# Kernel optimization log

Hardware: AMD Instinct MI355X
Metric: run time of the kernel (lower is better)

Reference implementation:

```python
import jax, jax.numpy as jnp
import numpy as np

H = 4      # n_heads
HD = 32    # head_dim
D = 128    # pair channels = H*HD
S = 384    # sequence length
EPS = 1e-5


def setup_inputs() -> dict:
    key = jax.random.key(0)
    ks = jax.random.split(key, 8)
    return {
        "x": jax.random.normal(ks[0], (1, S, S, D), dtype=jnp.float32),
        "attn_mask": jnp.zeros((1, 1, 1, S), dtype=jnp.float32),
        "ln_w": jax.random.uniform(ks[1], (D,), dtype=jnp.float32),
        "ln_b": jax.random.normal(ks[2], (D,), dtype=jnp.float32) * 0.02,
        "bias_w": jax.random.normal(ks[3], (H, D), dtype=jnp.float32) * 0.02,
        "qkv_w": jax.random.normal(ks[4], (3 * H * HD, D), dtype=jnp.float32) * 0.02,
        "g_w": jax.random.normal(ks[5], (H * HD, D), dtype=jnp.float32) * 0.02,
        "o_w": jax.random.normal(ks[6], (D, H * HD), dtype=jnp.float32) * 0.02,
    }


def reference(x, attn_mask, ln_w, ln_b, bias_w, qkv_w, g_w, o_w):
    # x: [1, S, S, D]; ending=False -> no permute
    xs = x[0]  # [S, S, D]; first S = batch of rows, second S = attended axis
    mu = jnp.mean(xs, axis=-1, keepdims=True)
    var = jnp.mean(jnp.square(xs - mu), axis=-1, keepdims=True)
    ln = (xs - mu) * jax.lax.rsqrt(var + EPS) * ln_w + ln_b  # [S, S, D]

    # triangle bias: D -> H, shaped [1, H, S, S], broadcast over row-batch
    bias = jnp.einsum('ijd,hd->hij', ln, bias_w)  # [H, S, S]

    # fused qkv projection, split heads
    qkv = jnp.einsum('bsd,ed->bse', ln, qkv_w)  # [S, S, 3*H*HD]
    q, k, v = jnp.split(qkv, 3, axis=-1)
    def heads(t):
        return t.reshape(S, S, H, HD).transpose(0, 2, 1, 3)  # [S, H, S, HD]
    q, k, v = heads(q), heads(k), heads(v)

    scale = 1.0 / jnp.sqrt(jnp.float32(HD))
    scores = jnp.einsum('bhqd,bhkd->bhqk', q, k) * scale  # [S, H, S, S]
    scores = scores + bias[None] + attn_mask  # attn_mask broadcasts [1,1,1,S]
    attn = jax.nn.softmax(scores, axis=-1)
    o = jnp.einsum('bhqk,bhkd->bhqd', attn, v)  # [S, H, S, HD]
    o = o.transpose(0, 2, 1, 3).reshape(S, S, H * HD)  # concat heads

    g = jnp.einsum('bsd,ed->bse', ln, g_w)  # [S, S, H*HD]
    o = o * jax.nn.sigmoid(g)
    out = jnp.einsum('bse,de->bsd', o, o_w)  # [S, S, D]
    return out[None]  # [1, S, S, D]
```

## Files before the change

kernel.cpp:

```cpp
#include <hip/hip_runtime.h>
#include <hip/hip_bf16.h>


#define S_ 384
#define D_ 128
#define MTOT (S_*S_)

typedef __bf16 bf16;
typedef __bf16 bf16x8 __attribute__((ext_vector_type(8)));
typedef __bf16 bf16x4 __attribute__((ext_vector_type(4)));
typedef float  f32x4  __attribute__((ext_vector_type(4)));

#define LOG2E      1.4426950408889634f
#define QSCALE     0.17677669529663687f
#define QSCALE_L2E 0.25505008455121566f

#if defined(__has_builtin)
#  if __has_builtin(__builtin_amdgcn_exp2f)
#    define HAVE_EXP2 1
#  else
#    define HAVE_EXP2 0
#  endif
#else
#  define HAVE_EXP2 0
#endif

#if HAVE_EXP2
#  define BIAS_MUL LOG2E
#  define Q_MUL    QSCALE_L2E
__device__ __forceinline__ float fast_pexp(float x) { return __builtin_amdgcn_exp2f(x); }
#else
#  define BIAS_MUL 1.0f
#  define Q_MUL    QSCALE
__device__ __forceinline__ float fast_pexp(float x) { return __expf(x); }
#endif

#define OFF_LN   0u
#define OFF_Q    37748736u
#define OFF_K    75497472u
#define OFF_V    113246208u
#define OFF_G    150994944u
#define OFF_BIAS 188743680u
#define OFF_W2   191102976u
#define OFF_OWB  191234048u

__global__ __launch_bounds__(256) void k0_convert(const float* __restrict__ qkv_w,
                                                  const float* __restrict__ g_w,
                                                  const float* __restrict__ o_w,
                                                  bf16* __restrict__ W2,
                                                  bf16* __restrict__ o_wb) {
    int idx = blockIdx.x * 256 + threadIdx.x;
    if (idx < 512 * 128) {
        float v = (idx < 384 * 128) ? qkv_w[idx] : g_w[idx - 384 * 128];
        W2[idx] = (bf16)v;
    }
    int idx2 = idx - 512 * 128;
    if (idx2 >= 0 && idx2 < 128 * 128) o_wb[idx2] = (bf16)o_w[idx2];
}

__global__ __launch_bounds__(256) void k1_ln(const float* __restrict__ x,
                                             const float* __restrict__ ln_w,
                                             const float* __restrict__ ln_b,
                                             const float* __restrict__ bias_w,
                                             const float* __restrict__ mask,
                                             bf16* __restrict__ ln_ws,
                                             float* __restrict__ bias_f) {
    int wid = threadIdx.x >> 6, lane = threadIdx.x & 63;
    int grp = lane >> 5, sub = lane & 31;
    int pos = blockIdx.x * 8 + wid * 2 + grp;
    f32x4 v = ((const f32x4*)(x + (size_t)pos * D_))[sub];
    float sum = v[0] + v[1] + v[2] + v[3];
    float ssq = v[0]*v[0] + v[1]*v[1] + v[2]*v[2] + v[3]*v[3];
    #pragma unroll
    for (int off = 16; off; off >>= 1) {
        sum += __shfl_xor(sum, off);
        ssq += __shfl_xor(ssq, off);
    }
    float mu   = sum * (1.0f / D_);
    float var  = ssq * (1.0f / D_) - mu * mu;
    float rstd = rsqrtf(var + 1e-5f);
    f32x4 w4 = ((const f32x4*)ln_w)[sub];
    f32x4 b4 = ((const f32x4*)ln_b)[sub];
    f32x4 y;
    #pragma unroll
    for (int i = 0; i < 4; ++i) y[i] = (v[i] - mu) * rstd * w4[i] + b4[i];
    bf16x4 yb;
    #pragma unroll
    for (int i = 0; i < 4; ++i) yb[i] = (bf16)y[i];
    *(bf16x4*)(ln_ws + (size_t)pos * D_ + 4 * sub) = yb;

    int ii = pos / S_, jj = pos - ii * S_;
    float mk = mask[jj];
    float p[4];
    #pragma unroll
    for (int h = 0; h < 4; ++h) {
        f32x4 bw = ((const f32x4*)(bias_w + h * D_))[sub];
        p[h] = y[0]*bw[0] + y[1]*bw[1] + y[2]*bw[2] + y[3]*bw[3];
    }
    #pragma unroll
    for (int off = 16; off; off >>= 1)
        #pragma unroll
        for (int h = 0; h < 4; ++h) p[h] += __shfl_xor(p[h], off);
    if (sub == 0) {
        int base = ((ii >> 4) * 24 + (jj >> 4)) * 256 + (((jj >> 2) & 3) * 16 + (ii & 15)) * 4 + (jj & 3);
        #pragma unroll
        for (int h = 0; h < 4; ++h)
            bias_f[h * 147456 + base] = (p[h] + mk) * BIAS_MUL;
    }
}

__global__ __launch_bounds__(512, 2) void k2_proj(const bf16* __restrict__ ln_ws,
                                                  const bf16* __restrict__ W2,
                                                  bf16* __restrict__ q_ws,
                                                  bf16* __restrict__ k_ws,
                                                  bf16* __restrict__ v_ws,
                                                  bf16* __restrict__ g_ws) {
    __shared__ __align__(16) char smem[128 * 272 + 128 * 272];
    char* As = smem;
    char* Bs = smem + 128 * 272;
    char* Cs = smem;
    int t = threadIdx.x;
    int bid = blockIdx.x;
    int xcd = bid & 7;
    int rem = bid >> 3;
    int by  = rem & 3;
    int bx  = ((rem >> 2) << 3) + xcd;
    int m0 = bx * 128;
    int n0 = by * 128;
    #pragma unroll
    for (int it = 0; it < 4; ++it) {
        int byte = it * 8192 + t * 16;
        int row = byte >> 8, colb = byte & 255;
        *(int4*)(As + row * 272 + colb) = *(const int4*)((const char*)ln_ws + (size_t)(m0 + row) * 256 + colb);
    }
    #pragma unroll
    for (int it = 0; it < 4; ++it) {
        int byte = it * 8192 + t * 16;
        int row = byte >> 8, colb = byte & 255;
        *(int4*)(Bs + row * 272 + colb) = *(const int4*)((const char*)W2 + (size_t)(n0 + row) * 256 + colb);
    }
    __syncthreads();
    int wid = t >> 6, lane = t & 63, lr = lane & 15, g = lane >> 4;
    int wm = wid >> 1, wn = wid & 1;
    f32x4 acc[2][4] = {};
    #pragma unroll
    for (int ks = 0; ks < 4; ++ks) {
        bf16x8 af[2], bfr[4];
        #pragma unroll
        for (int mt = 0; mt < 2; ++mt)
            af[mt] = *(const bf16x8*)(As + (wm * 32 + mt * 16 + lr) * 272 + ks * 64 + g * 16);
        #pragma unroll
        for (int nt = 0; nt < 4; ++nt)
            bfr[nt] = *(const bf16x8*)(Bs + (wn * 64 + nt * 16 + lr) * 272 + ks * 64 + g * 16);
        #pragma unroll
        for (int mt = 0; mt < 2; ++mt)
            #pragma unroll
            for (int nt = 0; nt < 4; ++nt)
                acc[mt][nt] = __builtin_amdgcn_mfma_f32_16x16x32_bf16(af[mt], bfr[nt], acc[mt][nt], 0, 0, 0);
    }
    __syncthreads();
    float cmul = (by == 0) ? Q_MUL : 1.0f;
    #pragma unroll
    for (int mt = 0; mt < 2; ++mt)
        #pragma unroll
        for (int nt = 0; nt < 4; ++nt)
            #pragma unroll
            for (int i = 0; i < 4; ++i) {
                int ml = wm * 32 + mt * 16 + g * 4 + i;
                int nl = wn * 64 + nt * 16 + lr;
                *(bf16*)(Cs + ml * 272 + nl * 2) = (bf16)(acc[mt][nt][i] * cmul);
            }
    __syncthreads();
    int b = m0 / 384;
    int jj0 = m0 - b * 384;
    if (by < 2) {
        bf16* dst0 = (by == 0) ? q_ws : k_ws;
        int h = wid >> 1, thalf = wid & 1;
        size_t bh = (size_t)b * 4 + h;
        bf16* dst = dst0 + bh * 12288 + (size_t)((jj0 >> 4) + thalf * 4) * 512 + lane * 8;
        #pragma unroll
        for (int tl = 0; tl < 4; ++tl) {
            bf16x8 v8 = *(const bf16x8*)(Cs + (thalf * 64 + tl * 16 + lr) * 272 + (h * 32 + 8 * g) * 2);
            *(bf16x8*)(dst + tl * 512) = v8;
        }
    } else if (by == 2) {
        int h = wid >> 1, vhalf = wid & 1;
        size_t bh = (size_t)b * 4 + h;
        bf16* dst = v_ws + bh * 12288 + (size_t)(jj0 >> 5) * 1024 + lane * 8;
        #pragma unroll
        for (int f = 0; f < 4; ++f) {
            int kt64 = vhalf * 2 + (f >> 1), dt = f & 1;
            bf16x8 v8;
            #pragma unroll
            for (int j = 0; j < 8; ++j) {
                int kl = 16 * (j >> 2) + 4 * g + (j & 3);
                v8[j] = *(const bf16*)(Cs + (kt64 * 32 + kl) * 272 + (h * 32 + dt * 16 + lr) * 2);
            }
            *(bf16x8*)(dst + kt64 * 1024 + dt * 512) = v8;
        }
    } else {
        #pragma unroll
        for (int j = 0; j < 4; ++j) {
            int byte = j * 8192 + t * 16;
            int ml = byte >> 8, col = byte & 255;
            *(int4*)((char*)g_ws + (size_t)(m0 + ml) * 256 + col) = *(const int4*)(Cs + ml * 272 + col);
        }
    }
}

__global__ __launch_bounds__(512, 3) void k3_attn(const bf16* __restrict__ q_ws,
                                                  const bf16* __restrict__ k_ws,
                                                  const bf16* __restrict__ v_ws,
                                                  const float* __restrict__ bias_f,
                                                  bf16* __restrict__ o_ws) {
    __shared__ __align__(16) char smem[49152];
    char* Ksh = smem;
    char* Vsh = smem + 24576;
    int t = threadIdx.x;
    int bh = blockIdx.x;
    int b = bh >> 2, h = bh & 3;
    const char* kbase = (const char*)(k_ws + (size_t)bh * 12288);
    const char* vbase = (const char*)(v_ws + (size_t)bh * 12288);
    #pragma unroll
    for (int it = 0; it < 3; ++it) {
        int byte = it * 8192 + t * 16;
        *(int4*)(Ksh + byte) = *(const int4*)(kbase + byte);
        *(int4*)(Vsh + byte) = *(const int4*)(vbase + byte);
    }
    __syncthreads();
    int wid = t >> 6, lane = t & 63, lr = lane & 15, g = lane >> 4;
    const char* qbase = (const char*)(q_ws + (size_t)bh * 12288);
    const float* bbase = bias_f + (size_t)h * 147456;
    bf16x8 qf[3];
    const f32x4* bp[3];
    #pragma unroll
    for (int u = 0; u < 3; ++u) {
        int qtile = wid + u * 8;
        qf[u] = *(const bf16x8*)(qbase + qtile * 1024 + lane * 16);
        bp[u] = (const f32x4*)(bbase + qtile * 6144) + lane;
    }
    f32x4 bcur[3][2];
    #pragma unroll
    for (int u = 0; u < 3; ++u) {
        bcur[u][0] = bp[u][0];
        bcur[u][1] = bp[u][64];
    }
    f32x4 oa[3][2] = {};
    float lsum[3] = {0.f, 0.f, 0.f};
    #pragma unroll 1
    for (int kt = 0; kt < 4; ++kt) {
        #pragma unroll
        for (int tt = 0; tt < 3; ++tt) {
            int k0t = kt * 6 + tt * 2;
            int knext = k0t + 2;
            f32x4 bnext[3][2];
            #pragma unroll
            for (int u = 0; u < 3; ++u) {
                bnext[u][0] = bp[u][knext * 64];
                bnext[u][1] = bp[u][(knext + 1) * 64];
            }
            bf16x8 kf0 = *(const bf16x8*)(Ksh + k0t * 1024 + lane * 16);
            bf16x8 kf1 = *(const bf16x8*)(Ksh + (k0t + 1) * 1024 + lane * 16);
            bf16x8 pf[3];
            #pragma unroll
            for (int u = 0; u < 3; ++u) {
                f32x4 a0 = __builtin_amdgcn_mfma_f32_16x16x32_bf16(kf0, qf[u], bcur[u][0], 0, 0, 0);
                f32x4 a1 = __builtin_amdgcn_mfma_f32_16x16x32_bf16(kf1, qf[u], bcur[u][1], 0, 0, 0);
                #pragma unroll
                for (int i = 0; i < 4; ++i) {
                    float p0 = fast_pexp(a0[i]);
                    float p1 = fast_pexp(a1[i]);
                    lsum[u] += p0 + p1;
                    pf[u][i]     = (bf16)p0;
                    pf[u][4 + i] = (bf16)p1;
                }
            }
            const char* vb = Vsh + (kt * 3 + tt) * 2048 + lane * 16;
            bf16x8 vf0 = *(const bf16x8*)(vb);
            bf16x8 vf1 = *(const bf16x8*)(vb + 1024);
            #pragma unroll
            for (int u = 0; u < 3; ++u) {
                oa[u][0] = __builtin_amdgcn_mfma_f32_16x16x32_bf16(pf[u], vf0, oa[u][0], 0, 0, 0);
                oa[u][1] = __builtin_amdgcn_mfma_f32_16x16x32_bf16(pf[u], vf1, oa[u][1], 0, 0, 0);
            }
            #pragma unroll
            for (int u = 0; u < 3; ++u) {
                bcur[u][0] = bnext[u][0];
                bcur[u][1] = bnext[u][1];
            }
        }
    }
    #pragma unroll
    for (int u = 0; u < 3; ++u) {
        float l = lsum[u];
        l += __shfl_xor(l, 16);
        l += __shfl_xor(l, 32);
        float inv = 1.0f / l;
        float invq[4];
        #pragma unroll
        for (int i = 0; i < 4; ++i) invq[i] = __shfl(inv, 4 * g + i);
        int q0 = (wid + u * 8) * 16;
        #pragma unroll
        for (int dt = 0; dt < 2; ++dt)
            #pragma unroll
            for (int i = 0; i < 4; ++i)
                o_ws[((size_t)b * 384 + q0 + 4 * g + i) * 128 + h * 32 + dt * 16 + lr] = (bf16)(oa[u][dt][i] * invq[i]);
    }
}

__global__ __launch_bounds__(512, 2) void k4_out(const bf16* __restrict__ o_ws,
                                                 const bf16* __restrict__ g_ws,
                                                 const bf16* __restrict__ o_wb,
                                                 float* __restrict__ out) {
    __shared__ __align__(16) char smem[128 * 272 + 128 * 272];
    char* As = smem;
    char* Bs = smem + 128 * 272;
    int t = threadIdx.x;
    int m0 = blockIdx.x * 128;
    #pragma unroll
    for (int it = 0; it < 4; ++it) {
        int byte = it * 8192 + t * 16;
        int row = byte >> 8, colb = byte & 255;
        bf16x8 o8 = *(const bf16x8*)((const char*)o_ws + (size_t)(m0 + row) * 256 + colb);
        bf16x8 g8 = *(const bf16x8*)((const char*)g_ws + (size_t)(m0 + row) * 256 + colb);
        bf16x8 a8;
        #pragma unroll
        for (int j = 0; j < 8; ++j) {
            float ov = (float)o8[j], gv = (float)g8[j];
            a8[j] = (bf16)(ov / (1.0f + __expf(-gv)));
        }
        *(bf16x8*)(As + row * 272 + colb) = a8;
    }
    #pragma unroll
    for (int it = 0; it < 4; ++it) {
        int byte = it * 8192 + t * 16;
        int row = byte >> 8, colb = byte & 255;
        *(int4*)(Bs + row * 272 + colb) = *(const int4*)((const char*)o_wb + (size_t)row * 256 + colb);
    }
    __syncthreads();
    int wid = t >> 6, lane = t & 63, lr = lane & 15, g = lane >> 4;
    int wm = wid >> 1, wn = wid & 1;
    f32x4 acc[2][4] = {};
    #pragma unroll
    for (int ks = 0; ks < 4; ++ks) {
        bf16x8 af[2], bfr[4];
        #pragma unroll
        for (int mt = 0; mt < 2; ++mt)
            af[mt] = *(const bf16x8*)(As + (wm * 32 + mt * 16 + lr) * 272 + ks * 64 + g * 16);
        #pragma unroll
        for (int nt = 0; nt < 4; ++nt)
            bfr[nt] = *(const bf16x8*)(Bs + (wn * 64 + nt * 16 + lr) * 272 + ks * 64 + g * 16);
        #pragma unroll
        for (int mt = 0; mt < 2; ++mt)
            #pragma unroll
            for (int nt = 0; nt < 4; ++nt)
                acc[mt][nt] = __builtin_amdgcn_mfma_f32_16x16x32_bf16(af[mt], bfr[nt], acc[mt][nt], 0, 0, 0);
    }
    #pragma unroll
    for (int mt = 0; mt < 2; ++mt)
        #pragma unroll
        for (int nt = 0; nt < 4; ++nt)
            #pragma unroll
            for (int i = 0; i < 4; ++i) {
                int m = m0 + wm * 32 + mt * 16 + g * 4 + i;
                int n = wn * 64 + nt * 16 + lr;
                out[(size_t)m * 128 + n] = acc[mt][nt][i];
            }
}

extern "C" void kernel_launch(void* const* d_in, const int* in_sizes, int n_in,
                              void* d_out, int out_size, void* d_ws, size_t ws_size,
                              hipStream_t stream) {
    const float* x      = (const float*)d_in[0];
    const float* mask   = (const float*)d_in[1];
    const float* ln_w   = (const float*)d_in[2];
    const float* ln_b   = (const float*)d_in[3];
    const float* bias_w = (const float*)d_in[4];
    const float* qkv_w  = (const float*)d_in[5];
    const float* g_w    = (const float*)d_in[6];
    const float* o_w    = (const float*)d_in[7];
    char* ws = (char*)d_ws;
    bf16*  ln_ws  = (bf16*)(ws + OFF_LN);
    bf16*  q_ws   = (bf16*)(ws + OFF_Q);
    bf16*  k_ws   = (bf16*)(ws + OFF_K);
    bf16*  v_ws   = (bf16*)(ws + OFF_V);
    bf16*  g_ws   = (bf16*)(ws + OFF_G);
    float* bias_f = (float*)(ws + OFF_BIAS);
    bf16*  W2     = (bf16*)(ws + OFF_W2);
    bf16*  o_wb   = (bf16*)(ws + OFF_OWB);
    bf16*  o_ws   = ln_ws;
    float* out    = (float*)d_out;

    k0_convert<<<dim3(320), dim3(256), 0, stream>>>(qkv_w, g_w, o_w, W2, o_wb);
    k1_ln<<<dim3(MTOT / 8), dim3(256), 0, stream>>>(x, ln_w, ln_b, bias_w, mask, ln_ws, bias_f);
    k2_proj<<<dim3(MTOT / 128 * 4), dim3(512), 0, stream>>>(ln_ws, W2, q_ws, k_ws, v_ws, g_ws);
    k3_attn<<<dim3(S_ * 4), dim3(512), 0, stream>>>(q_ws, k_ws, v_ws, bias_f, o_ws);
    k4_out<<<dim3(MTOT / 128), dim3(512), 0, stream>>>(o_ws, g_ws, o_wb, out);
}
```

Before: 163.0 us.

## Pre-swizzle weights into MFMA fragment order and read B operands from global

```diff
diff --git a/kernel.cpp b/kernel.cpp
--- a/kernel.cpp
+++ b/kernel.cpp
@@ -44,6 +44,10 @@
 #define OFF_W2   191102976u
 #define OFF_OWB  191234048u
 
+__device__ __forceinline__ int wfrag_idx(int n, int c) {
+    return (n >> 4) * 2048 + (c >> 5) * 512 + (16 * ((c >> 3) & 3) + (n & 15)) * 8 + (c & 7);
+}
+
 __global__ __launch_bounds__(256) void k0_convert(const float* __restrict__ qkv_w,
                                                   const float* __restrict__ g_w,
                                                   const float* __restrict__ o_w,
@@ -52,10 +56,11 @@
     int idx = blockIdx.x * 256 + threadIdx.x;
     if (idx < 512 * 128) {
         float v = (idx < 384 * 128) ? qkv_w[idx] : g_w[idx - 384 * 128];
-        W2[idx] = (bf16)v;
+        W2[wfrag_idx(idx >> 7, idx & 127)] = (bf16)v;
     }
     int idx2 = idx - 512 * 128;
-    if (idx2 >= 0 && idx2 < 128 * 128) o_wb[idx2] = (bf16)o_w[idx2];
+    if (idx2 >= 0 && idx2 < 128 * 128)
+        o_wb[wfrag_idx(idx2 >> 7, idx2 & 127)] = (bf16)o_w[idx2];
 }
 
 __global__ __launch_bounds__(256) void k1_ln(const float* __restrict__ x,
@@ -109,15 +114,14 @@
     }
 }
 
-__global__ __launch_bounds__(512, 2) void k2_proj(const bf16* __restrict__ ln_ws,
+__global__ __launch_bounds__(512, 3) void k2_proj(const bf16* __restrict__ ln_ws,
                                                   const bf16* __restrict__ W2,
                                                   bf16* __restrict__ q_ws,
                                                   bf16* __restrict__ k_ws,
                                                   bf16* __restrict__ v_ws,
                                                   bf16* __restrict__ g_ws) {
-    __shared__ __align__(16) char smem[128 * 272 + 128 * 272];
+    __shared__ __align__(16) char smem[128 * 272];
     char* As = smem;
-    char* Bs = smem + 128 * 272;
     char* Cs = smem;
     int t = threadIdx.x;
     int bid = blockIdx.x;
@@ -126,22 +130,16 @@
     int by  = rem & 3;
     int bx  = ((rem >> 2) << 3) + xcd;
     int m0 = bx * 128;
-    int n0 = by * 128;
     #pragma unroll
     for (int it = 0; it < 4; ++it) {
         int byte = it * 8192 + t * 16;
         int row = byte >> 8, colb = byte & 255;
         *(int4*)(As + row * 272 + colb) = *(const int4*)((const char*)ln_ws + (size_t)(m0 + row) * 256 + colb);
     }
-    #pragma unroll
-    for (int it = 0; it < 4; ++it) {
-        int byte = it * 8192 + t * 16;
-        int row = byte >> 8, colb = byte & 255;
-        *(int4*)(Bs + row * 272 + colb) = *(const int4*)((const char*)W2 + (size_t)(n0 + row) * 256 + colb);
-    }
     __syncthreads();
     int wid = t >> 6, lane = t & 63, lr = lane & 15, g = lane >> 4;
     int wm = wid >> 1, wn = wid & 1;
+    const char* wbase = (const char*)W2 + (size_t)(by * 8 + wn * 4) * 4096 + lane * 16;
     f32x4 acc[2][4] = {};
     #pragma unroll
     for (int ks = 0; ks < 4; ++ks) {
@@ -151,7 +149,7 @@
             af[mt] = *(const bf16x8*)(As + (wm * 32 + mt * 16 + lr) * 272 + ks * 64 + g * 16);
         #pragma unroll
         for (int nt = 0; nt < 4; ++nt)
-            bfr[nt] = *(const bf16x8*)(Bs + (wn * 64 + nt * 16 + lr) * 272 + ks * 64 + g * 16);
+            bfr[nt] = *(const bf16x8*)(wbase + nt * 4096 + ks * 1024);
         #pragma unroll
         for (int mt = 0; mt < 2; ++mt)
             #pragma unroll
@@ -308,13 +306,12 @@
     }
 }
 
-__global__ __launch_bounds__(512, 2) void k4_out(const bf16* __restrict__ o_ws,
+__global__ __launch_bounds__(512, 3) void k4_out(const bf16* __restrict__ o_ws,
                                                  const bf16* __restrict__ g_ws,
                                                  const bf16* __restrict__ o_wb,
                                                  float* __restrict__ out) {
-    __shared__ __align__(16) char smem[128 * 272 + 128 * 272];
+    __shared__ __align__(16) char smem[128 * 272];
     char* As = smem;
-    char* Bs = smem + 128 * 272;
     int t = threadIdx.x;
     int m0 = blockIdx.x * 128;
     #pragma unroll
@@ -331,15 +328,10 @@
         }
         *(bf16x8*)(As + row * 272 + colb) = a8;
     }
-    #pragma unroll
-    for (int it = 0; it < 4; ++it) {
-        int byte = it * 8192 + t * 16;
-        int row = byte >> 8, colb = byte & 255;
-        *(int4*)(Bs + row * 272 + colb) = *(const int4*)((const char*)o_wb + (size_t)row * 256 + colb);
-    }
     __syncthreads();
     int wid = t >> 6, lane = t & 63, lr = lane & 15, g = lane >> 4;
     int wm = wid >> 1, wn = wid & 1;
+    const char* wbase = (const char*)o_wb + (size_t)(wn * 4) * 4096 + lane * 16;
     f32x4 acc[2][4] = {};
     #pragma unroll
     for (int ks = 0; ks < 4; ++ks) {
@@ -349,7 +341,7 @@
             af[mt] = *(const bf16x8*)(As + (wm * 32 + mt * 16 + lr) * 272 + ks * 64 + g * 16);
         #pragma unroll
         for (int nt = 0; nt < 4; ++nt)
-            bfr[nt] = *(const bf16x8*)(Bs + (wn * 64 + nt * 16 + lr) * 272 + ks * 64 + g * 16);
+            bfr[nt] = *(const bf16x8*)(wbase + nt * 4096 + ks * 1024);
         #pragma unroll
         for (int mt = 0; mt < 2; ++mt)
             #pragma unroll
```

Result: slower. 168.7 us (+3.5%).
